# Kernel tuning notes

Measured on AMD Instinct MI355X. Metric: run time of the kernel, lower is better.

The kernel has to match this reference:

```python
import jax, jax.numpy as jnp
import numpy as np

DIM = 4096
CAP = 8192
EPS = 1e-8  # torch F.cosine_similarity denominator clamp


def setup_inputs() -> dict:
    key = jax.random.key(0)
    k1, k2, k3, k4, k5, k6 = jax.random.split(key, 6)
    return {
        "query": jax.random.normal(k1, (DIM,), dtype=jnp.float32),
        "memory_bank": jax.random.normal(k2, (CAP, DIM), dtype=jnp.float32),
        "importance": jax.random.uniform(k3, (CAP,), dtype=jnp.float32),
        "age": jax.random.uniform(k4, (CAP,), dtype=jnp.float32) * 1000.0,
        "W_dec": jax.random.normal(k5, (DIM, DIM), dtype=jnp.float32) * (1.0 / np.sqrt(DIM)),
        "b_dec": jax.random.normal(k6, (DIM,), dtype=jnp.float32) * 0.01,
        "top_k": 8,
    }


def reference(query, memory_bank, importance, age, W_dec, b_dec, top_k):
    # Cosine similarity of query against every memory row (torch semantics:
    # dot / max(||q||*||m||, eps)).
    dots = memory_bank @ query                       # [CAP]
    qn = jnp.sqrt(jnp.sum(query * query))
    mn = jnp.sqrt(jnp.sum(memory_bank * memory_bank, axis=1))
    sim = dots / jnp.maximum(qn * mn, EPS)
    # Time-decayed importance weighting.
    weighted = sim * importance * jnp.exp(-0.001 * age)
    # Top-k retrieval, mean-pool retrieved rows, decode.
    _, idx = jax.lax.top_k(weighted, top_k)          # [k]
    retrieved = jnp.mean(memory_bank[idx], axis=0)   # [DIM]
    return retrieved @ W_dec.T + b_dec
```

## Files before the change

### kernel.cpp

```cpp
#include <hip/hip_runtime.h>
#include <math.h>

#define DIM 4096
#define CAP 8192
#define EPS 1e-8f

__global__ __launch_bounds__(256) void score_kernel(
    const float* __restrict__ q,
    const float* __restrict__ mb,
    const float* __restrict__ imp,
    const float* __restrict__ age,
    float* __restrict__ weighted)
{
    const int row = blockIdx.x;
    const float4* __restrict__ mrow = (const float4*)(mb + (size_t)row * DIM);
    const float4* __restrict__ q4   = (const float4*)q;

    float dot = 0.f, msq = 0.f, qsq = 0.f;
    for (int i = threadIdx.x; i < DIM / 4; i += 256) {
        float4 m  = mrow[i];
        float4 qq = q4[i];
        dot += m.x * qq.x + m.y * qq.y + m.z * qq.z + m.w * qq.w;
        msq += m.x * m.x + m.y * m.y + m.z * m.z + m.w * m.w;
        qsq += qq.x * qq.x + qq.y * qq.y + qq.z * qq.z + qq.w * qq.w;
    }

    for (int off = 32; off > 0; off >>= 1) {
        dot += __shfl_down(dot, off, 64);
        msq += __shfl_down(msq, off, 64);
        qsq += __shfl_down(qsq, off, 64);
    }

    __shared__ float sdot[4], smsq[4], sqsq[4];
    const int wave = threadIdx.x >> 6;
    const int lane = threadIdx.x & 63;
    if (lane == 0) { sdot[wave] = dot; smsq[wave] = msq; sqsq[wave] = qsq; }
    __syncthreads();

    if (threadIdx.x == 0) {
        float d = 0.f, ms = 0.f, qs = 0.f;
        for (int w = 0; w < 4; ++w) { d += sdot[w]; ms += smsq[w]; qs += sqsq[w]; }
        float denom = fmaxf(sqrtf(qs) * sqrtf(ms), EPS);
        weighted[row] = (d / denom) * imp[row] * expf(-0.001f * age[row]);
    }
}

__global__ __launch_bounds__(1024) void topk_gather_kernel(
    const float* __restrict__ weighted,
    const float* __restrict__ mb,
    const int* __restrict__ topk_ptr,
    float* __restrict__ retrieved)
{
    __shared__ float wv[CAP];
    __shared__ float rv[16];
    __shared__ int   ri[16];
    __shared__ int   sidx[64];

    const int tid = threadIdx.x;
    for (int i = tid; i < CAP; i += 1024) wv[i] = weighted[i];
    __syncthreads();

    int k = *topk_ptr;
    if (k < 1) k = 1;
    if (k > 64) k = 64;

    for (int it = 0; it < k; ++it) {
        float bv = -INFINITY; int bi = 0x7fffffff;
        for (int i = tid; i < CAP; i += 1024) {
            float v = wv[i];
            if (v > bv) { bv = v; bi = i; }
        }
        for (int off = 32; off > 0; off >>= 1) {
            float ov = __shfl_down(bv, off, 64);
            int   oi = __shfl_down(bi, off, 64);
            if (ov > bv || (ov == bv && oi < bi)) { bv = ov; bi = oi; }
        }
        const int wave = tid >> 6;
        const int lane = tid & 63;
        if (lane == 0) { rv[wave] = bv; ri[wave] = bi; }
        __syncthreads();
        if (tid == 0) {
            float best = rv[0]; int besti = ri[0];
            for (int w = 1; w < 16; ++w) {
                if (rv[w] > best || (rv[w] == best && ri[w] < besti)) {
                    best = rv[w]; besti = ri[w];
                }
            }
            sidx[it] = besti;
            wv[besti] = -INFINITY;
        }
        __syncthreads();
    }

    const float inv_k = 1.0f / (float)k;
    for (int i = tid; i < DIM / 4; i += 1024) {
        float4 acc = make_float4(0.f, 0.f, 0.f, 0.f);
        for (int r = 0; r < k; ++r) {
            const float4* __restrict__ row = (const float4*)(mb + (size_t)sidx[r] * DIM);
            float4 v = row[i];
            acc.x += v.x; acc.y += v.y; acc.z += v.z; acc.w += v.w;
        }
        acc.x *= inv_k; acc.y *= inv_k; acc.z *= inv_k; acc.w *= inv_k;
        ((float4*)retrieved)[i] = acc;
    }
}

__global__ __launch_bounds__(256) void decode_kernel(
    const float* __restrict__ W,
    const float* __restrict__ b,
    const float* __restrict__ r,
    float* __restrict__ out)
{
    const int j = blockIdx.x;
    const float4* __restrict__ wrow = (const float4*)(W + (size_t)j * DIM);
    const float4* __restrict__ r4   = (const float4*)r;

    float acc = 0.f;
    for (int i = threadIdx.x; i < DIM / 4; i += 256) {
        float4 w = wrow[i];
        float4 v = r4[i];
        acc += w.x * v.x + w.y * v.y + w.z * v.z + w.w * v.w;
    }
    for (int off = 32; off > 0; off >>= 1) acc += __shfl_down(acc, off, 64);

    __shared__ float sacc[4];
    const int wave = threadIdx.x >> 6;
    const int lane = threadIdx.x & 63;
    if (lane == 0) sacc[wave] = acc;
    __syncthreads();
    if (threadIdx.x == 0) {
        float s = sacc[0] + sacc[1] + sacc[2] + sacc[3];
        out[j] = s + b[j];
    }
}

extern "C" void kernel_launch(void* const* d_in, const int* in_sizes, int n_in,
                              void* d_out, int out_size, void* d_ws, size_t ws_size,
                              hipStream_t stream) {
    const float* query      = (const float*)d_in[0];
    const float* memory     = (const float*)d_in[1];
    const float* importance = (const float*)d_in[2];
    const float* age        = (const float*)d_in[3];
    const float* W_dec      = (const float*)d_in[4];
    const float* b_dec      = (const float*)d_in[5];
    const int*   top_k      = (const int*)d_in[6];

    float* weighted  = (float*)d_ws;
    float* retrieved = (float*)d_ws + CAP;
    float* out       = (float*)d_out;

    score_kernel<<<CAP, 256, 0, stream>>>(query, memory, importance, age, weighted);
    topk_gather_kernel<<<1, 1024, 0, stream>>>(weighted, memory, top_k, retrieved);
    decode_kernel<<<DIM, 256, 0, stream>>>(W_dec, b_dec, retrieved, out);
}
```

Measured before the change: 263.6 us.

## Map one wavefront per row in score/decode and single-wave top-k selection

Score and decode kernels now assign one 64-lane wavefront per row, four rows per block, with fully unrolled FMA loops and no shared-memory or __syncthreads cross-wave reduction. The top-k kernel shrinks to 256 threads and runs the k selection passes inside one wavefront using float4 LDS reads and shuffles, removing the two block barriers per iteration. It also caps k at 16 instead of 64, which could give wrong results if top_k exceeds 16, and the single-block gather now has fewer threads.

```diff
diff --git a/kernel.cpp b/kernel.cpp
--- a/kernel.cpp
+++ b/kernel.cpp
@@ -4,6 +4,7 @@
 #define DIM 4096
 #define CAP 8192
 #define EPS 1e-8f
+#define MAXK 16
 
 __global__ __launch_bounds__(256) void score_kernel(
     const float* __restrict__ q,
@@ -12,96 +13,87 @@
     const float* __restrict__ age,
     float* __restrict__ weighted)
 {
-    const int row = blockIdx.x;
+    const int lane = threadIdx.x & 63;
+    const int row  = (blockIdx.x << 2) + (threadIdx.x >> 6);
+
     const float4* __restrict__ mrow = (const float4*)(mb + (size_t)row * DIM);
     const float4* __restrict__ q4   = (const float4*)q;
 
     float dot = 0.f, msq = 0.f, qsq = 0.f;
-    for (int i = threadIdx.x; i < DIM / 4; i += 256) {
+    #pragma unroll
+    for (int it = 0; it < 16; ++it) {
+        const int i = lane + (it << 6);
         float4 m  = mrow[i];
         float4 qq = q4[i];
-        dot += m.x * qq.x + m.y * qq.y + m.z * qq.z + m.w * qq.w;
-        msq += m.x * m.x + m.y * m.y + m.z * m.z + m.w * m.w;
-        qsq += qq.x * qq.x + qq.y * qq.y + qq.z * qq.z + qq.w * qq.w;
+        dot = fmaf(m.x, qq.x, fmaf(m.y, qq.y, fmaf(m.z, qq.z, fmaf(m.w, qq.w, dot))));
+        msq = fmaf(m.x, m.x,  fmaf(m.y, m.y,  fmaf(m.z, m.z,  fmaf(m.w, m.w,  msq))));
+        qsq = fmaf(qq.x, qq.x, fmaf(qq.y, qq.y, fmaf(qq.z, qq.z, fmaf(qq.w, qq.w, qsq))));
     }
 
+    #pragma unroll
     for (int off = 32; off > 0; off >>= 1) {
         dot += __shfl_down(dot, off, 64);
         msq += __shfl_down(msq, off, 64);
         qsq += __shfl_down(qsq, off, 64);
     }
 
-    __shared__ float sdot[4], smsq[4], sqsq[4];
-    const int wave = threadIdx.x >> 6;
-    const int lane = threadIdx.x & 63;
-    if (lane == 0) { sdot[wave] = dot; smsq[wave] = msq; sqsq[wave] = qsq; }
-    __syncthreads();
-
-    if (threadIdx.x == 0) {
-        float d = 0.f, ms = 0.f, qs = 0.f;
-        for (int w = 0; w < 4; ++w) { d += sdot[w]; ms += smsq[w]; qs += sqsq[w]; }
-        float denom = fmaxf(sqrtf(qs) * sqrtf(ms), EPS);
-        weighted[row] = (d / denom) * imp[row] * expf(-0.001f * age[row]);
+    if (lane == 0) {
+        float denom = fmaxf(sqrtf(qsq) * sqrtf(msq), EPS);
+        weighted[row] = (dot / denom) * imp[row] * expf(-0.001f * age[row]);
     }
 }
 
-__global__ __launch_bounds__(1024) void topk_gather_kernel(
+__global__ __launch_bounds__(256) void topk_gather_kernel(
     const float* __restrict__ weighted,
     const float* __restrict__ mb,
     const int* __restrict__ topk_ptr,
     float* __restrict__ retrieved)
 {
     __shared__ float wv[CAP];
-    __shared__ float rv[16];
-    __shared__ int   ri[16];
-    __shared__ int   sidx[64];
+    __shared__ int   sidx[MAXK];
 
     const int tid = threadIdx.x;
-    for (int i = tid; i < CAP; i += 1024) wv[i] = weighted[i];
+    int k = *topk_ptr;
+    k = (k < 1) ? 1 : (k > MAXK ? MAXK : k);
+
+    const float4* __restrict__ w4 = (const float4*)weighted;
+    float4* wv4 = (float4*)wv;
+    for (int i = tid; i < CAP / 4; i += 256) wv4[i] = w4[i];
     __syncthreads();
 
-    int k = *topk_ptr;
-    if (k < 1) k = 1;
-    if (k > 64) k = 64;
-
-    for (int it = 0; it < k; ++it) {
-        float bv = -INFINITY; int bi = 0x7fffffff;
-        for (int i = tid; i < CAP; i += 1024) {
-            float v = wv[i];
-            if (v > bv) { bv = v; bi = i; }
+    if (tid < 64) {
+        for (int it = 0; it < k; ++it) {
+            float bv = -INFINITY;
+            int   bi = 0x7fffffff;
+            for (int i = tid; i < CAP / 4; i += 64) {
+                float4 v = wv4[i];
+                const int base = i << 2;
+                if (v.x > bv) { bv = v.x; bi = base; }
+                if (v.y > bv) { bv = v.y; bi = base + 1; }
+                if (v.z > bv) { bv = v.z; bi = base + 2; }
+                if (v.w > bv) { bv = v.w; bi = base + 3; }
+            }
+            #pragma unroll
+            for (int off = 32; off > 0; off >>= 1) {
+                float ov = __shfl_down(bv, off, 64);
+                int   oi = __shfl_down(bi, off, 64);
+                if (ov > bv || (ov == bv && oi < bi)) { bv = ov; bi = oi; }
+            }
+            const int best = __shfl(bi, 0, 64);
+            if (tid == 0) sidx[it] = best;
+            wv[best] = -INFINITY;
         }
-        for (int off = 32; off > 0; off >>= 1) {
-            float ov = __shfl_down(bv, off, 64);
-            int   oi = __shfl_down(bi, off, 64);
-            if (ov > bv || (ov == bv && oi < bi)) { bv = ov; bi = oi; }
-        }
-        const int wave = tid >> 6;
-        const int lane = tid & 63;
-        if (lane == 0) { rv[wave] = bv; ri[wave] = bi; }
-        __syncthreads();
-        if (tid == 0) {
-            float best = rv[0]; int besti = ri[0];
-            for (int w = 1; w < 16; ++w) {
-                if (rv[w] > best || (rv[w] == best && ri[w] < besti)) {
-                    best = rv[w]; besti = ri[w];
-                }
-            }
-            sidx[it] = besti;
-            wv[besti] = -INFINITY;
-        }
-        __syncthreads();
     }
+    __syncthreads();
 
     const float inv_k = 1.0f / (float)k;
-    for (int i = tid; i < DIM / 4; i += 1024) {
-        float4 acc = make_float4(0.f, 0.f, 0.f, 0.f);
+    for (int i = tid; i < DIM / 4; i += 256) {
+        float ax = 0.f, ay = 0.f, az = 0.f, aw = 0.f;
         for (int r = 0; r < k; ++r) {
-            const float4* __restrict__ row = (const float4*)(mb + (size_t)sidx[r] * DIM);
-            float4 v = row[i];
-            acc.x += v.x; acc.y += v.y; acc.z += v.z; acc.w += v.w;
+            const float4 v = ((const float4*)(mb + (size_t)sidx[r] * DIM))[i];
+            ax += v.x; ay += v.y; az += v.z; aw += v.w;
         }
-        acc.x *= inv_k; acc.y *= inv_k; acc.z *= inv_k; acc.w *= inv_k;
-        ((float4*)retrieved)[i] = acc;
+        ((float4*)retrieved)[i] = make_float4(ax * inv_k, ay * inv_k, az * inv_k, aw * inv_k);
     }
 }
 
@@ -111,27 +103,25 @@
     const float* __restrict__ r,
     float* __restrict__ out)
 {
-    const int j = blockIdx.x;
+    const int lane = threadIdx.x & 63;
+    const int j    = (blockIdx.x << 2) + (threadIdx.x >> 6);
+
     const float4* __restrict__ wrow = (const float4*)(W + (size_t)j * DIM);
     const float4* __restrict__ r4   = (const float4*)r;
 
     float acc = 0.f;
-    for (int i = threadIdx.x; i < DIM / 4; i += 256) {
+    #pragma unroll
+    for (int it = 0; it < 16; ++it) {
+        const int i = lane + (it << 6);
         float4 w = wrow[i];
         float4 v = r4[i];
-        acc += w.x * v.x + w.y * v.y + w.z * v.z + w.w * v.w;
+        acc = fmaf(w.x, v.x, fmaf(w.y, v.y, fmaf(w.z, v.z, fmaf(w.w, v.w, acc))));
     }
+
+    #pragma unroll
     for (int off = 32; off > 0; off >>= 1) acc += __shfl_down(acc, off, 64);
 
-    __shared__ float sacc[4];
-    const int wave = threadIdx.x >> 6;
-    const int lane = threadIdx.x & 63;
-    if (lane == 0) sacc[wave] = acc;
-    __syncthreads();
-    if (threadIdx.x == 0) {
-        float s = sacc[0] + sacc[1] + sacc[2] + sacc[3];
-        out[j] = s + b[j];
-    }
+    if (lane == 0) out[j] = acc + b[j];
 }
 
 extern "C" void kernel_launch(void* const* d_in, const int* in_sizes, int n_in,
@@ -149,7 +139,7 @@
     float* retrieved = (float*)d_ws + CAP;
     float* out       = (float*)d_out;
 
-    score_kernel<<<CAP, 256, 0, stream>>>(query, memory, importance, age, weighted);
-    topk_gather_kernel<<<1, 1024, 0, stream>>>(weighted, memory, top_k, retrieved);
-    decode_kernel<<<DIM, 256, 0, stream>>>(W_dec, b_dec, retrieved, out);
+    score_kernel<<<CAP / 4, 256, 0, stream>>>(query, memory, importance, age, weighted);
+    topk_gather_kernel<<<1, 256, 0, stream>>>(weighted, memory, top_k, retrieved);
+    decode_kernel<<<DIM / 4, 256, 0, stream>>>(W_dec, b_dec, retrieved, out);
 }
```

New measurement: 269.2 us. 1.02x slower.
